# Performance work log

Hardware: AMD Instinct MI355X
Metric: run time of the kernel (lower is better)

The kernel has to match this reference:

```python
import jax, jax.numpy as jnp
import numpy as np

PRE_NMS_THRESH = 0.05
PRE_NMS_TOP_N = 1000
NMS_THRESH = 0.6
FPN_POST_NMS_TOP_N = 100
MIN_SIZE = 0.0
NUM_CLASSES = 80
BBOX_W = (10.0, 10.0, 5.0, 5.0)
SCALE_CLAMP = float(np.log(1000.0 / 16.0))
CLASS_OFFSET = 2000.0  # > max image coordinate after clipping
N_IMG = 16
LEVELS = [(100, 152, 8, 64), (50, 76, 16, 128), (25, 38, 32, 256), (13, 19, 64, 512), (7, 10, 128, 1024)]


def _make_anchors(H, W, stride, size):
    cx = np.arange(W, dtype=np.float32) * stride
    cy = np.arange(H, dtype=np.float32) * stride
    xx, yy = np.meshgrid(cx, cy)
    ctr = np.stack([xx, yy, xx, yy], -1).reshape(-1, 4)
    base = np.array([-size / 2.0, -size / 2.0, size / 2.0, size / 2.0], np.float32)
    return jnp.asarray((ctr + base).astype(np.float32))


def setup_inputs() -> dict:
    key = jax.random.key(0)
    ks = jax.random.split(key, 10)
    inp = {}
    for i, (H, W, st, sz) in enumerate(LEVELS):
        inp[f"cls{i}"] = jax.random.normal(ks[i], (N_IMG, NUM_CLASSES, H, W), jnp.float32) * 2.0 - 4.0
        inp[f"reg{i}"] = jax.random.normal(ks[5 + i], (N_IMG, 4, H, W), jnp.float32)
        inp[f"anc{i}"] = _make_anchors(H, W, st, sz)
    inp["image_sizes"] = jnp.tile(jnp.array([[800, 1216]], jnp.int32), (N_IMG, 1))
    return inp


def _decode(deltas, anchors):
    wx, wy, ww, wh = BBOX_W
    w = anchors[..., 2] - anchors[..., 0] + 1.0
    h = anchors[..., 3] - anchors[..., 1] + 1.0
    cx = anchors[..., 0] + 0.5 * w
    cy = anchors[..., 1] + 0.5 * h
    dx = deltas[..., 0] / wx
    dy = deltas[..., 1] / wy
    dw = jnp.minimum(deltas[..., 2] / ww, SCALE_CLAMP)
    dh = jnp.minimum(deltas[..., 3] / wh, SCALE_CLAMP)
    pcx = dx * w + cx
    pcy = dy * h + cy
    pw = jnp.exp(dw) * w
    ph = jnp.exp(dh) * h
    return jnp.stack([pcx - 0.5 * (pw - 1.0), pcy - 0.5 * (ph - 1.0),
                      pcx + 0.5 * (pw - 1.0), pcy + 0.5 * (ph - 1.0)], -1)


def _level(cls, reg, anc):
    n, C, H, W = cls.shape  # A = 1
    scores = jax.nn.sigmoid(jnp.transpose(cls, (0, 2, 3, 1)).reshape(n, -1, C))  # [n, HW, C]
    regf = jnp.transpose(reg, (0, 2, 3, 1)).reshape(n, -1, 4)  # [n, HW, 4]
    flat = scores.reshape(n, -1)
    masked = jnp.where(flat > PRE_NMS_THRESH, flat, 0.0)
    vals, idx = jax.lax.top_k(masked, PRE_NMS_TOP_N)  # emulates thresh + per-image clamp
    loc = idx // C
    cl = idx % C
    deltas = jnp.take_along_axis(regf, loc[..., None], axis=1)  # [n, K, 4]
    boxes = _decode(deltas, anc[loc])
    valid = vals > PRE_NMS_THRESH
    sc = jnp.where(valid, jnp.sqrt(jnp.maximum(vals, 1e-12)), 0.0)
    return boxes, sc, cl, valid


def _nms_keep(boxes, classes, valid):
    M = boxes.shape[0]
    b = boxes + classes.astype(boxes.dtype)[:, None] * CLASS_OFFSET  # class-aware offsets
    areas = (b[:, 2] - b[:, 0]) * (b[:, 3] - b[:, 1])
    ar = jnp.arange(M)

    def body(i, sup):
        bi = b[i]
        xx1 = jnp.maximum(bi[0], b[:, 0])
        yy1 = jnp.maximum(bi[1], b[:, 1])
        xx2 = jnp.minimum(bi[2], b[:, 2])
        yy2 = jnp.minimum(bi[3], b[:, 3])
        inter = jnp.maximum(xx2 - xx1, 0.0) * jnp.maximum(yy2 - yy1, 0.0)
        iou = inter / (areas[i] + areas - inter + 1e-9)
        new = sup | ((iou > NMS_THRESH) & (ar > i))
        return jnp.where(sup[i], sup, new)

    sup = jax.lax.fori_loop(0, M, body, ~valid)
    return ~sup


def _forward(cls_l, reg_l, anc_l, image_sizes):
    outs = [_level(c, r, a) for c, r, a in zip(cls_l, reg_l, anc_l)]
    boxes = jnp.concatenate([o[0] for o in outs], 1)   # [N, M, 4]
    scores = jnp.concatenate([o[1] for o in outs], 1)  # [N, M]
    classes = jnp.concatenate([o[2] for o in outs], 1)
    valid = jnp.concatenate([o[3] for o in outs], 1)
    hs = image_sizes[:, 0:1].astype(boxes.dtype)
    ws = image_sizes[:, 1:2].astype(boxes.dtype)
    x1 = jnp.clip(boxes[..., 0], 0.0, ws)
    y1 = jnp.clip(boxes[..., 1], 0.0, hs)
    x2 = jnp.clip(boxes[..., 2], 0.0, ws)
    y2 = jnp.clip(boxes[..., 3], 0.0, hs)
    boxes = jnp.stack([x1, y1, x2, y2], -1)
    nonempty = ((x2 - x1) > MIN_SIZE) & ((y2 - y1) > MIN_SIZE)
    valid = valid & nonempty
    scores = jnp.where(valid, scores, 0.0)
    order = jnp.argsort(-scores, axis=1)
    boxes = jnp.take_along_axis(boxes, order[..., None], 1)
    scores = jnp.take_along_axis(scores, order, 1)
    classes = jnp.take_along_axis(classes, order, 1)
    valid = jnp.take_along_axis(valid, order, 1)
    keep = jax.vmap(_nms_keep)(boxes, classes, valid)
    fs = jnp.where(keep, scores, 0.0)
    top_scores, idx = jax.lax.top_k(fs, FPN_POST_NMS_TOP_N)  # kthvalue filter == top-k
    top_boxes = jnp.take_along_axis(boxes, idx[..., None], 1)
    top_classes = jnp.take_along_axis(classes, idx, 1)
    return top_boxes, top_scores, top_classes


def reference(cls0, cls1, cls2, cls3, cls4, reg0, reg1, reg2, reg3, reg4,
              anc0, anc1, anc2, anc3, anc4, image_sizes):
    return _forward([cls0, cls1, cls2, cls3, cls4],
                    [reg0, reg1, reg2, reg3, reg4],
                    [anc0, anc1, anc2, anc3, anc4], image_sizes)
```

## Files before the change

kernel.cpp:

```cpp
#include <hip/hip_runtime.h>
#include <stdint.h>
#include <math.h>

#define NLEV 5
#define NIMG 16
#define NCLS 80
#define TOPK 1000
#define MTOT 5000
#define LPAD 1024
#define BNDCAP 4096
#define NBINS 288
#define BIN0 7846
#define OUTK 100
#define CHUNK 8192
#define NCHUNK 3216
#define CCAND 1024
#define ROWCAP 8192
#define CCAP 512

__device__ __constant__ int c_HW[NLEV]   = {15200, 3800, 950, 247, 70};
__device__ __constant__ int c_E[NLEV]    = {1216000, 304000, 76000, 19760, 5600};
__device__ __constant__ int c_cpr[NLEV]  = {149, 38, 10, 3, 1};
__device__ __constant__ int c_cbase[NLEV + 1] = {0, 2384, 2992, 3152, 3200, 3216};
__device__ __constant__ int c_GB[NLEV]   = {256, 230, 179, 64, 0};

struct Params {
    const float* cls[NLEV];
    const float* reg[NLEV];
    const float* anc[NLEV];
    const int* imsize;
};

__device__ inline void decode_entry(const Params& P, int img, int lvl, uint32_t idx,
                                    float bclip[4], int* cls_out, bool* nonempty) {
    int HW = c_HW[lvl];
    int loc = (int)idx / NCLS;
    int c = (int)idx - loc * NCLS;
    const float* a = P.anc[lvl] + 4 * loc;
    float a0 = a[0], a1 = a[1], a2 = a[2], a3 = a[3];
    const float* rg = P.reg[lvl] + (size_t)img * 4 * HW + loc;
    float d0 = rg[0], d1 = rg[HW], d2 = rg[2 * HW], d3 = rg[3 * HW];
    float w = a2 - a0 + 1.0f, h = a3 - a1 + 1.0f;
    float cx = a0 + 0.5f * w, cy = a1 + 0.5f * h;
    float dx = d0 / 10.0f, dy = d1 / 10.0f;
    const float SCALE_CLAMP = 4.135166556742356f;
    float dw = fminf(d2 / 5.0f, SCALE_CLAMP);
    float dh = fminf(d3 / 5.0f, SCALE_CLAMP);
    float pcx = dx * w + cx, pcy = dy * h + cy;
    float pw = (float)exp((double)dw) * w;
    float ph = (float)exp((double)dh) * h;
    float x1 = pcx - 0.5f * (pw - 1.0f), y1 = pcy - 0.5f * (ph - 1.0f);
    float x2 = pcx + 0.5f * (pw - 1.0f), y2 = pcy + 0.5f * (ph - 1.0f);
    float Hs = (float)P.imsize[img * 2 + 0];
    float Ws = (float)P.imsize[img * 2 + 1];
    float x1c = fminf(fmaxf(x1, 0.0f), Ws);
    float y1c = fminf(fmaxf(y1, 0.0f), Hs);
    float x2c = fminf(fmaxf(x2, 0.0f), Ws);
    float y2c = fminf(fmaxf(y2, 0.0f), Hs);
    bclip[0] = x1c; bclip[1] = y1c; bclip[2] = x2c; bclip[3] = y2c;
    *cls_out = c;
    *nonempty = ((x2c - x1c) > 0.0f) && ((y2c - y1c) > 0.0f);
}

__device__ inline float sigmoid_f(float x) {
    return (float)(1.0 / (1.0 + exp(-(double)x)));
}

__device__ inline uint32_t f2o(float f) {
    uint32_t b = __float_as_uint(f);
    return (b & 0x80000000u) ? ~b : (b | 0x80000000u);
}
__device__ inline float o2f(uint32_t o) {
    uint32_t b = (o & 0x80000000u) ? (o & 0x7FFFFFFFu) : ~o;
    return __uint_as_float(b);
}

__device__ inline void chunk_map(int bid, int* lvl, int* img, int* start, int* end) {
    int l = 0;
#pragma unroll
    for (int q = 1; q < NLEV; q++) if (bid >= c_cbase[q]) l = q;
    int r = bid - c_cbase[l];
    int cpr = c_cpr[l];
    int im = r / cpr;
    int ch = r - im * cpr;
    int E = c_E[l];
    int st = ch * CHUNK;
    *lvl = l; *img = im; *start = st; *end = min(st + CHUNK, E);
}

__global__ __launch_bounds__(320) void k_thr(float* T, uint32_t* hist, uint32_t* cnts) {
    int b = blockIdx.x;
    int t = threadIdx.x;
    if (t < NBINS) hist[b * NBINS + t] = 0;
    if (b == 1 && t < 240) cnts[t] = 0;
    if (b == 0 && t < NBINS) {
        uint32_t lo = f2o(-4.0f), hi = f2o(20.0f);
        while (hi - lo > 1u) {
            uint32_t mid = lo + ((hi - lo) >> 1);
            float xm = o2f(mid);
            float s = sigmoid_f(xm);
            bool pass = (s > 0.05f) && (((int)(__float_as_uint(s) >> 17) - BIN0) >= t);
            if (pass) hi = mid; else lo = mid;
        }
        float xr = o2f(hi);
        float sv = sigmoid_f(xr);
        bool ok = (sv > 0.05f) && (((int)(__float_as_uint(sv) >> 17) - BIN0) >= t);
        T[t] = ok ? xr : __uint_as_float(0x7F800000u);
    }
}

__global__ __launch_bounds__(256) void k_hist(Params P, const float* __restrict__ T,
                                              uint32_t* __restrict__ hist,
                                              uint64_t* __restrict__ rowCand,
                                              uint32_t* __restrict__ rowCnt,
                                              uint32_t* __restrict__ fbflag,
                                              uint32_t* __restrict__ histBad) {
    __shared__ uint32_t lh[NBINS];
    __shared__ float sT[NBINS];
    __shared__ uint64_t cand[CCAND];
    __shared__ uint32_t ccnt, wbase;
    int l, img, start, end;
    chunk_map(blockIdx.x, &l, &img, &start, &end);
    for (int b = threadIdx.x; b < NBINS; b += 256) { lh[b] = 0; sT[b] = T[b]; }
    if (threadIdx.x == 0) ccnt = 0;
    __syncthreads();
    float gthr = sT[c_GB[l]];
    int HW = c_HW[l];
    int row = l * NIMG + img;
    const float4* __restrict__ p = (const float4*)(P.cls[l] + (size_t)img * c_E[l] + start);
    int n4 = (end - start) >> 2;
    float4 r[8];
#pragma unroll
    for (int u = 0; u < 8; u++) {
        int f = u * 256 + threadIdx.x;
        r[u] = (f < n4) ? p[f] : make_float4(-1e30f, -1e30f, -1e30f, -1e30f);
    }
    __builtin_amdgcn_sched_barrier(0);
#pragma unroll
    for (int u = 0; u < 8; u++) {
        float4 x4 = r[u];
        float xs[4] = {x4.x, x4.y, x4.z, x4.w};
#pragma unroll
        for (int k = 0; k < 4; k++) {
            float xv = xs[k];
            if (xv >= gthr) {
                uint32_t lp = atomicAdd(&ccnt, 1u);
                if (lp < CCAND) {
                    uint32_t pos = (uint32_t)((u * 256 + threadIdx.x) * 4 + k);
                    cand[lp] = ((uint64_t)__float_as_uint(xv) << 32) | pos;
                }
            }
        }
    }
    __syncthreads();
    uint32_t cc = ccnt;
    uint32_t n = min(cc, (uint32_t)CCAND);
    if (threadIdx.x == 0) {
        wbase = atomicAdd(&rowCnt[row], n);
        if (cc > CCAND) { atomicOr(&fbflag[row], 1u); atomicOr(&histBad[row], 1u); }
        else if (wbase + n > ROWCAP) atomicOr(&fbflag[row], 1u);
    }
    __syncthreads();
    for (uint32_t i = threadIdx.x; i < n; i += 256) {
        uint64_t rec = cand[i];
        float xv = __uint_as_float((uint32_t)(rec >> 32));
        int pos = (int)(rec & 0xFFFFu);
        float se = 1.0f / (1.0f + __expf(-xv));
        int b = (int)(__float_as_uint(se) >> 17) - BIN0;
        b = min(max(b, 0), NBINS - 1);
        while (b > 0 && xv < sT[b]) b--;
        while (b + 1 < NBINS && xv >= sT[b + 1]) b++;
        atomicAdd(&lh[b], 1u);
        int q2 = start + pos;
        int c = q2 / HW;
        int pidx = q2 - c * HW;
        uint32_t idx = (uint32_t)(pidx * NCLS + c);
        uint32_t gpos = wbase + i;
        if (gpos < ROWCAP)
            rowCand[(size_t)row * ROWCAP + gpos] = ((uint64_t)__float_as_uint(xv) << 32) | idx;
    }
    __syncthreads();
    for (int b = threadIdx.x; b < NBINS; b += 256) {
        uint32_t c = lh[b];
        if (c) atomicAdd(&hist[row * NBINS + b], c);
    }
}

__global__ __launch_bounds__(1024) void k_selkr(Params P, const float* T,
                                                const uint32_t* hist,
                                                const uint64_t* rowCand, const uint32_t* rowCnt,
                                                const uint32_t* fbflag, const uint32_t* histBad,
                                                uint64_t* keys) {
    __shared__ uint64_t smain[1024];
    __shared__ uint64_t sbnd[BNDCAP];
    __shared__ uint64_t kk[LPAD];
    __shared__ uint32_t lhist[NBINS];
    __shared__ uint32_t cnt0, cnt1;
    __shared__ int s_B, s_cab, s_need, s_cum, s_fail;
    int blk = blockIdx.x;
    int img = blk / NLEV, lvl = blk - img * NLEV;
    int row = lvl * NIMG + img;
    int E = c_E[lvl];
    int HW = c_HW[lvl];
    if (threadIdx.x < NBINS) lhist[threadIdx.x] = hist[row * NBINS + threadIdx.x];
    if (threadIdx.x == 0) { cnt0 = 0; cnt1 = 0; s_fail = 0; }
    __syncthreads();
    if (threadIdx.x == 0) {
        int GBl = c_GB[lvl];
        int cum = 0, B = -3, need = 0, cab = 0;
        if (histBad[row] == 0) {
            for (int b = NBINS - 1; b >= GBl; b--) {
                int c = (int)lhist[b];
                if (cum + c >= TOPK) { B = b; cab = cum; need = TOPK - cum; break; }
                cum += c;
            }
        }
        if (B == -3) s_fail = 1;
        else { s_B = B; s_cab = cab; s_need = need; s_cum = cum; }
    }
    __syncthreads();
    if (s_fail) {
        float t0 = T[0];
        for (int b = threadIdx.x; b < NBINS; b += 1024) lhist[b] = 0;
        __syncthreads();
        const float* base = P.cls[lvl] + (size_t)img * E;
        for (int e = threadIdx.x; e < E; e += 1024) {
            float xv = base[e];
            if (xv >= t0) {
                float sc = sigmoid_f(xv);
                int b = (int)(__float_as_uint(sc) >> 17) - BIN0;
                b = min(max(b, 0), NBINS - 1);
                atomicAdd(&lhist[b], 1u);
            }
        }
        __syncthreads();
        if (threadIdx.x == 0) {
            int cum = 0, B = -1, need = 0, cab = 0;
            for (int b = NBINS - 1; b >= 0; b--) {
                int c = (int)lhist[b];
                if (cum + c >= TOPK) { B = b; cab = cum; need = TOPK - cum; break; }
                cum += c;
            }
            if (B < 0) { cab = cum; need = 0; }
            s_B = B; s_cab = cab; s_need = need; s_cum = cum;
        }
        __syncthreads();
    }
    int B = s_B, cab = s_cab, need = s_need, cum = s_cum;
    float xt = T[max(B, 0)];
    float tB1 = T[min(B + 1, NBINS - 1)];
    uint32_t rcnt = rowCnt[row];
    bool fb = (fbflag[row] != 0) || (rcnt > ROWCAP) || s_fail;
    if (!fb) {
        const uint64_t* rc = rowCand + (size_t)row * ROWCAP;
        int cntr = (int)rcnt;
        for (int i = threadIdx.x; i < cntr; i += 1024) {
            uint64_t rec = rc[i];
            float x = __uint_as_float((uint32_t)(rec >> 32));
            if (x >= tB1) {
                uint32_t lp = atomicAdd(&cnt0, 1u);
                if (lp < 1024) smain[lp] = rec;
            } else if (x >= xt) {
                uint32_t lp = atomicAdd(&cnt1, 1u);
                if (lp < BNDCAP) sbnd[lp] = rec;
            }
        }
    } else {
        const float* base = P.cls[lvl] + (size_t)img * E;
        for (int e = threadIdx.x; e < E; e += 1024) {
            float xv = base[e];
            if (xv >= xt) {
                int c = e / HW;
                int pidx = e - c * HW;
                uint32_t idx = (uint32_t)(pidx * NCLS + c);
                uint64_t rec = ((uint64_t)__float_as_uint(xv) << 32) | idx;
                if (xv >= tB1) {
                    uint32_t lp = atomicAdd(&cnt0, 1u);
                    if (lp < 1024) smain[lp] = rec;
                } else {
                    uint32_t lp = atomicAdd(&cnt1, 1u);
                    if (lp < BNDCAP) sbnd[lp] = rec;
                }
            }
        }
    }
    __syncthreads();
    int take = 0;
    int cnt = min((int)cnt1, BNDCAP);
    if (need > 0) {
        for (int i = threadIdx.x; i < cnt; i += 1024) {
            uint64_t r = sbnd[i];
            float x = __uint_as_float((uint32_t)(r >> 32));
            uint32_t sb = __float_as_uint(sigmoid_f(x));
            sbnd[i] = ((uint64_t)(uint32_t)(~sb) << 32) | (uint32_t)r;
        }
        __syncthreads();
        int N = 64; while (N < cnt) N <<= 1;
        for (int i = threadIdx.x; i < N; i += 1024) {
            if (i >= cnt) sbnd[i] = ~0ULL;
        }
        __syncthreads();
        for (int k = 2; k <= N; k <<= 1) {
            for (int j = k >> 1; j > 0; j >>= 1) {
                for (int i = threadIdx.x; i < N; i += 1024) {
                    int ixj = i ^ j;
                    if (ixj > i) {
                        uint64_t A = sbnd[i], Bv = sbnd[ixj];
                        bool up = ((i & k) == 0);
                        if (up ? (A > Bv) : (A < Bv)) { sbnd[i] = Bv; sbnd[ixj] = A; }
                    }
                }
                __syncthreads();
            }
        }
        take = min(need, cnt);
    }
    int nmain = min((int)cnt0, 1024);
    int filled = (B < 0) ? cum : (cab + take);
    for (int slot = threadIdx.x; slot < LPAD; slot += 1024) {
        uint64_t key;
        if (slot >= TOPK) key = ~0ULL;
        else {
            uint32_t bits = 0, idx = 0;
            if (slot < filled) {
                if (slot < cab || B < 0) {
                    if (slot < nmain) {
                        uint64_t r = smain[slot];
                        float x = __uint_as_float((uint32_t)(r >> 32));
                        bits = __float_as_uint(sigmoid_f(x));
                        idx = (uint32_t)r;
                    }
                } else {
                    uint64_t wv = sbnd[slot - cab];
                    bits = ~((uint32_t)(wv >> 32));
                    idx = (uint32_t)wv;
                }
            }
            uint32_t be = 0;
            if (bits != 0) {
                float bc[4]; int cc; bool ne;
                decode_entry(P, img, lvl, idx, bc, &cc, &ne);
                if (ne) be = bits;
            }
            key = ((uint64_t)(uint32_t)(~be) << 24) | ((uint64_t)lvl << 21) | (uint64_t)idx;
        }
        kk[slot] = key;
    }
    __syncthreads();
    for (int k = 2; k <= LPAD; k <<= 1) {
        for (int j = k >> 1; j > 0; j >>= 1) {
            for (int i = threadIdx.x; i < LPAD; i += 1024) {
                int ixj = i ^ j;
                if (ixj > i) {
                    uint64_t A = kk[i], Bv = kk[ixj];
                    bool up = ((i & k) == 0);
                    if (up ? (A > Bv) : (A < Bv)) { kk[i] = Bv; kk[ixj] = A; }
                }
            }
            __syncthreads();
        }
    }
    uint64_t* g = keys + (size_t)blk * LPAD;
    for (int i = threadIdx.x; i < LPAD; i += 1024) g[i] = kk[i];
}

__global__ __launch_bounds__(1024) void k_merge(Params P, const uint64_t* keys,
                                                float4* boff, float* area, float4* bclip,
                                                float* scs, int* clss,
                                                uint8_t* keepB, uint8_t* clsB) {
    __shared__ uint64_t sl[NLEV * LPAD];
    int img = blockIdx.x >> 2;
    int part = blockIdx.x & 3;
    const uint64_t* g = keys + (size_t)img * NLEV * LPAD;
    for (int i = threadIdx.x; i < NLEV * LPAD; i += 1024) sl[i] = g[i];
    __syncthreads();
    const int gb = img * MTOT;
    int e0 = part * (NLEV * LPAD / 4);
    int e1 = e0 + (NLEV * LPAD / 4);
    for (int e = e0 + threadIdx.x; e < e1; e += 1024) {
        int l = e >> 10, i = e & (LPAD - 1);
        if (i >= TOPK) continue;
        uint64_t K = sl[e];
        int rank = i;
#pragma unroll
        for (int l2 = 0; l2 < NLEV; l2++) {
            if (l2 == l) continue;
            const uint64_t* s2 = &sl[l2 << 10];
            int lo = 0, hi = TOPK;
            while (lo < hi) {
                int mid = (lo + hi) >> 1;
                if (s2[mid] < K) lo = mid + 1; else hi = mid;
            }
            rank += lo;
        }
        uint32_t bits = ~((uint32_t)(K >> 24));
        int lvl = (int)((K >> 21) & 7);
        uint32_t idx = (uint32_t)(K & 0x1FFFFF);
        float bc[4]; int cc; bool ne;
        decode_entry(P, img, lvl, idx, bc, &cc, &ne);
        float sc = 0.0f;
        if (bits != 0) {
            float s = __uint_as_float(bits);
            sc = sqrtf(fmaxf(s, 1e-12f));
        }
        float off = (float)cc * 2000.0f;
        float b0 = bc[0] + off, b1 = bc[1] + off, b2 = bc[2] + off, b3 = bc[3] + off;
        int t = gb + rank;
        boff[t] = make_float4(b0, b1, b2, b3);
        area[t] = (b2 - b0) * (b3 - b1);
        bclip[t] = make_float4(bc[0], bc[1], bc[2], bc[3]);
        scs[t] = sc;
        clss[t] = cc;
        keepB[t] = 0;
        clsB[t] = (sc != 0.0f) ? (uint8_t)cc : (uint8_t)0xFF;
    }
}

__global__ __launch_bounds__(64) void k_cnms(const float4* boff, const float* area,
                                             const uint8_t* clsB, uint8_t* keepB) {
    __shared__ float sx1[CCAP], sy1[CCAP], sx2[CCAP], sy2[CCAP], sar[CCAP];
    __shared__ uint16_t ranks[CCAP];
    int img = blockIdx.x / NCLS;
    int cls = blockIdx.x - img * NCLS;
    int lane = threadIdx.x;
    const int gb = img * MTOT;

    int n = 0;
    const uchar4* cp = (const uchar4*)(clsB + gb);
    for (int base = 0; base < 1250; base += 64) {
        int q = base + lane;
        uchar4 cv = (q < 1250) ? cp[q] : make_uchar4(255, 255, 255, 255);
#pragma unroll
        for (int b = 0; b < 4; b++) {
            int cb = (b == 0) ? cv.x : (b == 1) ? cv.y : (b == 2) ? cv.z : cv.w;
            bool pred = (cb == cls);
            uint64_t mask = __ballot(pred);
            int pos = n + (int)__popcll(mask & ((1ULL << lane) - 1ULL));
            if (pred && pos < CCAP) ranks[pos] = (uint16_t)(q * 4 + b);
            n += (int)__popcll(mask);
        }
    }
    n = min(n, CCAP);
    __syncthreads();
    if (n == 0) return;

    for (int i = lane; i < n; i += 64) {
        int t = ranks[i];
        float4 b = boff[gb + t];
        sx1[i] = b.x; sy1[i] = b.y; sx2[i] = b.z; sy2[i] = b.w;
        sar[i] = area[gb + t];
    }
    __syncthreads();

    uint64_t m[CCAP / 64];
#pragma unroll
    for (int c = 0; c < CCAP / 64; c++) m[c] = 0ULL;
#pragma unroll
    for (int c = 0; c < CCAP / 64; c++) {
        if (c * 64 >= n) break;
        for (int ii = 0; ii < 64; ii++) {
            int i = c * 64 + ii;
            if (i >= n) break;
            if ((m[c] >> ii) & 1ULL) continue;
            float bx1 = sx1[i], by1 = sy1[i], bx2 = sx2[i], by2 = sy2[i], bai = sar[i];
            if (lane == 0) keepB[gb + ranks[i]] = 1;
#pragma unroll
            for (int c2 = 0; c2 < CCAP / 64; c2++) {
                if (c2 < c) continue;
                if (c2 * 64 >= n) break;
                int j = c2 * 64 + lane;
                float xx1 = fmaxf(bx1, sx1[j]), yy1 = fmaxf(by1, sy1[j]);
                float xx2 = fminf(bx2, sx2[j]), yy2 = fminf(by2, sy2[j]);
                float inter = fmaxf(xx2 - xx1, 0.0f) * fmaxf(yy2 - yy1, 0.0f);
                float iou = inter / (bai + sar[j] - inter + 1e-9f);
                bool pr = (j > i) && (j < n) && (iou > 0.6f);
                m[c2] |= __ballot(pr);
            }
        }
    }
}

__global__ __launch_bounds__(64) void k_out(const float4* bclip, const float* scs,
                                            const int* clss, const uint8_t* keepB, float* out) {
    __shared__ int keptIdx[OUTK];
    int img = blockIdx.x;
    int lane = threadIdx.x;
    const int gb = img * MTOT;
    int kc = 0;
    for (int base = 0; base < MTOT && kc < OUTK; base += 64) {
        int t = base + lane;
        bool pred = (t < MTOT) && (keepB[gb + t] != 0);
        uint64_t mask = __ballot(pred);
        int pos = kc + (int)__popcll(mask & ((1ULL << lane) - 1ULL));
        if (pred && pos < OUTK) keptIdx[pos] = t;
        kc = min(kc + (int)__popcll(mask), OUTK);
    }
    for (int base = 0; base < MTOT && kc < OUTK; base += 64) {
        int t = base + lane;
        bool pred = (t < MTOT) && (keepB[gb + t] == 0);
        uint64_t mask = __ballot(pred);
        int pos = kc + (int)__popcll(mask & ((1ULL << lane) - 1ULL));
        if (pred && pos < OUTK) keptIdx[pos] = t | (1 << 30);
        kc = min(kc + (int)__popcll(mask), OUTK);
    }
    __syncthreads();
    for (int t = lane; t < OUTK; t += 64) {
        int ke = keptIdx[t];
        bool fil = (ke >> 30) & 1;
        int e = ke & 0x3FFFFFFF;
        float4 b = bclip[gb + e];
        out[((size_t)img * OUTK + t) * 4 + 0] = b.x;
        out[((size_t)img * OUTK + t) * 4 + 1] = b.y;
        out[((size_t)img * OUTK + t) * 4 + 2] = b.z;
        out[((size_t)img * OUTK + t) * 4 + 3] = b.w;
        out[NIMG * OUTK * 4 + img * OUTK + t] = fil ? 0.0f : scs[gb + e];
        out[NIMG * OUTK * 4 + NIMG * OUTK + img * OUTK + t] = (float)clss[gb + e];
    }
}

extern "C" void kernel_launch(void* const* d_in, const int* in_sizes, int n_in,
                              void* d_out, int out_size, void* d_ws, size_t ws_size,
                              hipStream_t stream) {
    Params P;
    for (int l = 0; l < 5; l++) {
        P.cls[l] = (const float*)d_in[l * 3 + 0];
        P.reg[l] = (const float*)d_in[l * 3 + 1];
        P.anc[l] = (const float*)d_in[l * 3 + 2];
    }
    P.imsize = (const int*)d_in[15];

    char* w = (char*)d_ws;
    uint64_t* rowCand  = (uint64_t*)(w + 0);
    float4*   boff     = (float4*)(w + 0);
    float*    area     = (float*)(w + 1280000);
    float4*   bclipb   = (float4*)(w + 1600000);
    float*    scs      = (float*)(w + 2880000);
    int*      clss     = (int*)(w + 3200000);
    float*    T        = (float*)(w + 5242880);
    uint32_t* hist     = (uint32_t*)(w + 5244032);
    uint32_t* rowCnt   = (uint32_t*)(w + 5336192);
    uint32_t* fbflag   = (uint32_t*)(w + 5336512);
    uint32_t* histBad  = (uint32_t*)(w + 5336832);
    uint64_t* keys     = (uint64_t*)(w + 5337152);
    uint8_t*  keepB    = (uint8_t*)(w + 5992512);
    uint8_t*  clsB     = (uint8_t*)(w + 6072512);

    k_thr<<<80, 320, 0, stream>>>(T, hist, rowCnt);
    k_hist<<<NCHUNK, 256, 0, stream>>>(P, T, hist, rowCand, rowCnt, fbflag, histBad);
    k_selkr<<<NIMG * NLEV, 1024, 0, stream>>>(P, T, hist, rowCand, rowCnt, fbflag, histBad, keys);
    k_merge<<<NIMG * 4, 1024, 0, stream>>>(P, keys, boff, area, bclipb, scs, clss, keepB, clsB);
    k_cnms<<<NIMG * NCLS, 64, 0, stream>>>(boff, area, clsB, keepB);
    k_out<<<NIMG, 64, 0, stream>>>(bclipb, scs, clss, keepB, (float*)d_out);
}
```

Measured before the change: 162.6 us.

## Fuse merge into select and output into NMS via last-block atomic counters

Merges k_merge into the tail of k_selkr and k_out into the tail of k_cnms. In each case the last block to finish, found with an atomic done counter, does the follow-on work, which removes two kernel launches and their gaps. The merge stage now runs in one block per image instead of four, so it has less parallelism. Per-level row capacities also shrink the candidate buffer, so the workspace layout is reshuffled to avoid aliasing with the box buffers.

Result: slower. 201.2 us (+23.8%).

```diff
diff --git a/kernel.cpp b/kernel.cpp
--- a/kernel.cpp
+++ b/kernel.cpp
@@ -15,7 +15,6 @@
 #define CHUNK 8192
 #define NCHUNK 3216
 #define CCAND 1024
-#define ROWCAP 8192
 #define CCAP 512
 
 __device__ __constant__ int c_HW[NLEV]   = {15200, 3800, 950, 247, 70};
@@ -23,6 +22,8 @@
 __device__ __constant__ int c_cpr[NLEV]  = {149, 38, 10, 3, 1};
 __device__ __constant__ int c_cbase[NLEV + 1] = {0, 2384, 2992, 3152, 3200, 3216};
 __device__ __constant__ int c_GB[NLEV]   = {256, 230, 179, 64, 0};
+__device__ __constant__ int c_rowCap[NLEV]  = {6144, 6144, 4096, 4096, 2048};
+__device__ __constant__ int c_rowBase[NLEV] = {0, 98304, 196608, 262144, 327680};
 
 struct Params {
     const float* cls[NLEV];
@@ -92,7 +93,7 @@
     int b = blockIdx.x;
     int t = threadIdx.x;
     if (t < NBINS) hist[b * NBINS + t] = 0;
-    if (b == 1 && t < 240) cnts[t] = 0;
+    if (b == 1 && t < 272) cnts[t] = 0;
     if (b == 0 && t < NBINS) {
         uint32_t lo = f2o(-4.0f), hi = f2o(20.0f);
         while (hi - lo > 1u) {
@@ -127,6 +128,8 @@
     float gthr = sT[c_GB[l]];
     int HW = c_HW[l];
     int row = l * NIMG + img;
+    uint32_t cap = (uint32_t)c_rowCap[l];
+    size_t rbase = (size_t)c_rowBase[l] + (size_t)img * cap;
     const float4* __restrict__ p = (const float4*)(P.cls[l] + (size_t)img * c_E[l] + start);
     int n4 = (end - start) >> 2;
     float4 r[8];
@@ -158,7 +161,7 @@
     if (threadIdx.x == 0) {
         wbase = atomicAdd(&rowCnt[row], n);
         if (cc > CCAND) { atomicOr(&fbflag[row], 1u); atomicOr(&histBad[row], 1u); }
-        else if (wbase + n > ROWCAP) atomicOr(&fbflag[row], 1u);
+        else if (wbase + n > cap) atomicOr(&fbflag[row], 1u);
     }
     __syncthreads();
     for (uint32_t i = threadIdx.x; i < n; i += 256) {
@@ -176,8 +179,8 @@
         int pidx = q2 - c * HW;
         uint32_t idx = (uint32_t)(pidx * NCLS + c);
         uint32_t gpos = wbase + i;
-        if (gpos < ROWCAP)
-            rowCand[(size_t)row * ROWCAP + gpos] = ((uint64_t)__float_as_uint(xv) << 32) | idx;
+        if (gpos < cap)
+            rowCand[rbase + gpos] = ((uint64_t)__float_as_uint(xv) << 32) | idx;
     }
     __syncthreads();
     for (int b = threadIdx.x; b < NBINS; b += 256) {
@@ -190,13 +193,17 @@
                                                 const uint32_t* hist,
                                                 const uint64_t* rowCand, const uint32_t* rowCnt,
                                                 const uint32_t* fbflag, const uint32_t* histBad,
-                                                uint64_t* keys) {
-    __shared__ uint64_t smain[1024];
-    __shared__ uint64_t sbnd[BNDCAP];
+                                                uint64_t* keys, uint32_t* imgDone,
+                                                float4* boff, float* area, float4* bclip,
+                                                float* scs, int* clss,
+                                                uint8_t* keepB, uint8_t* clsB) {
+    __shared__ uint64_t shpool[NLEV * LPAD];
     __shared__ uint64_t kk[LPAD];
     __shared__ uint32_t lhist[NBINS];
     __shared__ uint32_t cnt0, cnt1;
-    __shared__ int s_B, s_cab, s_need, s_cum, s_fail;
+    __shared__ int s_B, s_cab, s_need, s_cum, s_fail, s_win;
+    uint64_t* smain = shpool;
+    uint64_t* sbnd = shpool + 1024;
     int blk = blockIdx.x;
     int img = blk / NLEV, lvl = blk - img * NLEV;
     int row = lvl * NIMG + img;
@@ -249,10 +256,11 @@
     int B = s_B, cab = s_cab, need = s_need, cum = s_cum;
     float xt = T[max(B, 0)];
     float tB1 = T[min(B + 1, NBINS - 1)];
+    uint32_t cap = (uint32_t)c_rowCap[lvl];
     uint32_t rcnt = rowCnt[row];
-    bool fb = (fbflag[row] != 0) || (rcnt > ROWCAP) || s_fail;
+    bool fb = (fbflag[row] != 0) || (rcnt > cap) || s_fail;
     if (!fb) {
-        const uint64_t* rc = rowCand + (size_t)row * ROWCAP;
+        const uint64_t* rc = rowCand + (size_t)c_rowBase[lvl] + (size_t)img * cap;
         int cntr = (int)rcnt;
         for (int i = threadIdx.x; i < cntr; i += 1024) {
             uint64_t rec = rc[i];
@@ -362,29 +370,28 @@
     }
     uint64_t* g = keys + (size_t)blk * LPAD;
     for (int i = threadIdx.x; i < LPAD; i += 1024) g[i] = kk[i];
-}
-
-__global__ __launch_bounds__(1024) void k_merge(Params P, const uint64_t* keys,
-                                                float4* boff, float* area, float4* bclip,
-                                                float* scs, int* clss,
-                                                uint8_t* keepB, uint8_t* clsB) {
-    __shared__ uint64_t sl[NLEV * LPAD];
-    int img = blockIdx.x >> 2;
-    int part = blockIdx.x & 3;
-    const uint64_t* g = keys + (size_t)img * NLEV * LPAD;
-    for (int i = threadIdx.x; i < NLEV * LPAD; i += 1024) sl[i] = g[i];
+    __syncthreads();
+    __threadfence();
+    if (threadIdx.x == 0) {
+        uint32_t old = atomicAdd(&imgDone[img], 1u);
+        s_win = (old == NLEV - 1);
+    }
+    __syncthreads();
+    if (!s_win) return;
+    __threadfence();
+    uint64_t* sl = shpool;
+    const uint64_t* gk = keys + (size_t)img * NLEV * LPAD;
+    for (int i = threadIdx.x; i < NLEV * LPAD; i += 1024) sl[i] = gk[i];
     __syncthreads();
     const int gb = img * MTOT;
-    int e0 = part * (NLEV * LPAD / 4);
-    int e1 = e0 + (NLEV * LPAD / 4);
-    for (int e = e0 + threadIdx.x; e < e1; e += 1024) {
-        int l = e >> 10, i = e & (LPAD - 1);
+    for (int e = threadIdx.x; e < NLEV * LPAD; e += 1024) {
+        int lv = e >> 10, i = e & (LPAD - 1);
         if (i >= TOPK) continue;
         uint64_t K = sl[e];
         int rank = i;
 #pragma unroll
         for (int l2 = 0; l2 < NLEV; l2++) {
-            if (l2 == l) continue;
+            if (l2 == lv) continue;
             const uint64_t* s2 = &sl[l2 << 10];
             int lo = 0, hi = TOPK;
             while (lo < hi) {
@@ -394,10 +401,10 @@
             rank += lo;
         }
         uint32_t bits = ~((uint32_t)(K >> 24));
-        int lvl = (int)((K >> 21) & 7);
+        int klvl = (int)((K >> 21) & 7);
         uint32_t idx = (uint32_t)(K & 0x1FFFFF);
         float bc[4]; int cc; bool ne;
-        decode_entry(P, img, lvl, idx, bc, &cc, &ne);
+        decode_entry(P, img, klvl, idx, bc, &cc, &ne);
         float sc = 0.0f;
         if (bits != 0) {
             float s = __uint_as_float(bits);
@@ -417,9 +424,12 @@
 }
 
 __global__ __launch_bounds__(64) void k_cnms(const float4* boff, const float* area,
-                                             const uint8_t* clsB, uint8_t* keepB) {
+                                             const uint8_t* clsB, uint8_t* keepB,
+                                             const float4* bclip, const float* scs,
+                                             const int* clss, uint32_t* nmsDone, float* out) {
     __shared__ float sx1[CCAP], sy1[CCAP], sx2[CCAP], sy2[CCAP], sar[CCAP];
     __shared__ uint16_t ranks[CCAP];
+    __shared__ int keptIdx[OUTK];
     int img = blockIdx.x / NCLS;
     int cls = blockIdx.x - img * NCLS;
     int lane = threadIdx.x;
@@ -441,51 +451,46 @@
         }
     }
     n = min(n, CCAP);
-    __syncthreads();
-    if (n == 0) return;
-
-    for (int i = lane; i < n; i += 64) {
-        int t = ranks[i];
-        float4 b = boff[gb + t];
-        sx1[i] = b.x; sy1[i] = b.y; sx2[i] = b.z; sy2[i] = b.w;
-        sar[i] = area[gb + t];
-    }
-    __syncthreads();
-
-    uint64_t m[CCAP / 64];
-#pragma unroll
-    for (int c = 0; c < CCAP / 64; c++) m[c] = 0ULL;
-#pragma unroll
-    for (int c = 0; c < CCAP / 64; c++) {
-        if (c * 64 >= n) break;
-        for (int ii = 0; ii < 64; ii++) {
-            int i = c * 64 + ii;
-            if (i >= n) break;
-            if ((m[c] >> ii) & 1ULL) continue;
-            float bx1 = sx1[i], by1 = sy1[i], bx2 = sx2[i], by2 = sy2[i], bai = sar[i];
-            if (lane == 0) keepB[gb + ranks[i]] = 1;
-#pragma unroll
-            for (int c2 = 0; c2 < CCAP / 64; c2++) {
-                if (c2 < c) continue;
-                if (c2 * 64 >= n) break;
-                int j = c2 * 64 + lane;
-                float xx1 = fmaxf(bx1, sx1[j]), yy1 = fmaxf(by1, sy1[j]);
-                float xx2 = fminf(bx2, sx2[j]), yy2 = fminf(by2, sy2[j]);
-                float inter = fmaxf(xx2 - xx1, 0.0f) * fmaxf(yy2 - yy1, 0.0f);
-                float iou = inter / (bai + sar[j] - inter + 1e-9f);
-                bool pr = (j > i) && (j < n) && (iou > 0.6f);
-                m[c2] |= __ballot(pr);
-            }
-        }
-    }
-}
-
-__global__ __launch_bounds__(64) void k_out(const float4* bclip, const float* scs,
-                                            const int* clss, const uint8_t* keepB, float* out) {
-    __shared__ int keptIdx[OUTK];
-    int img = blockIdx.x;
-    int lane = threadIdx.x;
-    const int gb = img * MTOT;
+    if (n > 0) {
+        for (int i = lane; i < n; i += 64) {
+            int t = ranks[i];
+            float4 b = boff[gb + t];
+            sx1[i] = b.x; sy1[i] = b.y; sx2[i] = b.z; sy2[i] = b.w;
+            sar[i] = area[gb + t];
+        }
+        uint64_t m[CCAP / 64];
+#pragma unroll
+        for (int c = 0; c < CCAP / 64; c++) m[c] = 0ULL;
+#pragma unroll
+        for (int c = 0; c < CCAP / 64; c++) {
+            if (c * 64 >= n) break;
+            for (int ii = 0; ii < 64; ii++) {
+                int i = c * 64 + ii;
+                if (i >= n) break;
+                if ((m[c] >> ii) & 1ULL) continue;
+                float bx1 = sx1[i], by1 = sy1[i], bx2 = sx2[i], by2 = sy2[i], bai = sar[i];
+                if (lane == 0) keepB[gb + ranks[i]] = 1;
+#pragma unroll
+                for (int c2 = 0; c2 < CCAP / 64; c2++) {
+                    if (c2 < c) continue;
+                    if (c2 * 64 >= n) break;
+                    int j = c2 * 64 + lane;
+                    float xx1 = fmaxf(bx1, sx1[j]), yy1 = fmaxf(by1, sy1[j]);
+                    float xx2 = fminf(bx2, sx2[j]), yy2 = fminf(by2, sy2[j]);
+                    float inter = fmaxf(xx2 - xx1, 0.0f) * fmaxf(yy2 - yy1, 0.0f);
+                    float iou = inter / (bai + sar[j] - inter + 1e-9f);
+                    bool pr = (j > i) && (j < n) && (iou > 0.6f);
+                    m[c2] |= __ballot(pr);
+                }
+            }
+        }
+    }
+    __threadfence();
+    int old = 0;
+    if (lane == 0) old = (int)atomicAdd(&nmsDone[img], 1u);
+    old = __shfl(old, 0);
+    if (old != NCLS - 1) return;
+    __threadfence();
     int kc = 0;
     for (int base = 0; base < MTOT && kc < OUTK; base += 64) {
         int t = base + lane;
@@ -531,24 +536,28 @@
 
     char* w = (char*)d_ws;
     uint64_t* rowCand  = (uint64_t*)(w + 0);
-    float4*   boff     = (float4*)(w + 0);
-    float*    area     = (float*)(w + 1280000);
-    float4*   bclipb   = (float4*)(w + 1600000);
-    float*    scs      = (float*)(w + 2880000);
-    int*      clss     = (int*)(w + 3200000);
-    float*    T        = (float*)(w + 5242880);
-    uint32_t* hist     = (uint32_t*)(w + 5244032);
-    uint32_t* rowCnt   = (uint32_t*)(w + 5336192);
-    uint32_t* fbflag   = (uint32_t*)(w + 5336512);
-    uint32_t* histBad  = (uint32_t*)(w + 5336832);
-    uint64_t* keys     = (uint64_t*)(w + 5337152);
-    uint8_t*  keepB    = (uint8_t*)(w + 5992512);
-    uint8_t*  clsB     = (uint8_t*)(w + 6072512);
-
-    k_thr<<<80, 320, 0, stream>>>(T, hist, rowCnt);
+    float4*   boff     = (float4*)(w + 2883584);
+    float*    area     = (float*)(w + 4163584);
+    float4*   bclipb   = (float4*)(w + 4483584);
+    float*    scs      = (float*)(w + 5763584);
+    int*      clss     = (int*)(w + 6083584);
+    float*    T        = (float*)(w + 6403584);
+    uint32_t* hist     = (uint32_t*)(w + 6404736);
+    uint32_t* cnts     = (uint32_t*)(w + 6496896);
+    uint32_t* rowCnt   = cnts;
+    uint32_t* fbflag   = cnts + 80;
+    uint32_t* histBad  = cnts + 160;
+    uint32_t* imgDone  = cnts + 240;
+    uint32_t* nmsDone  = cnts + 256;
+    uint64_t* keys     = (uint64_t*)(w + 6497984);
+    uint8_t*  keepB    = (uint8_t*)(w + 7153344);
+    uint8_t*  clsB     = (uint8_t*)(w + 7233344);
+
+    k_thr<<<80, 320, 0, stream>>>(T, hist, cnts);
     k_hist<<<NCHUNK, 256, 0, stream>>>(P, T, hist, rowCand, rowCnt, fbflag, histBad);
-    k_selkr<<<NIMG * NLEV, 1024, 0, stream>>>(P, T, hist, rowCand, rowCnt, fbflag, histBad, keys);
-    k_merge<<<NIMG * 4, 1024, 0, stream>>>(P, keys, boff, area, bclipb, scs, clss, keepB, clsB);
-    k_cnms<<<NIMG * NCLS, 64, 0, stream>>>(boff, area, clsB, keepB);
-    k_out<<<NIMG, 64, 0, stream>>>(bclipb, scs, clss, keepB, (float*)d_out);
-}
+    k_selkr<<<NIMG * NLEV, 1024, 0, stream>>>(P, T, hist, rowCand, rowCnt, fbflag, histBad,
+                                              keys, imgDone, boff, area, bclipb, scs, clss,
+                                              keepB, clsB);
+    k_cnms<<<NIMG * NCLS, 64, 0, stream>>>(boff, area, clsB, keepB, bclipb, scs, clss,
+                                           nmsDone, (float*)d_out);
+}
```
